# Kernel tuning notes

Hardware: AMD Instinct MI355X
Metric: run time of the kernel (lower is better)

## Reference

```python
import jax, jax.numpy as jnp
import numpy as np

B, NC, H, W = 8, 3, 24, 150
P = 2                      # patch size along time == sub_seq
WS = W // P                # 75 time segments per joint
N = H * WS                 # 1800 patches
PD = P * NC                # 6 time values per patch (time_values_per_joint)
D = 512                    # encoder_dim
L = 4                      # transformer depth
NH = 8
DH = D // NH
MLP = 4 * D
MASK_RATIO = 0.5
NM = int(MASK_RATIO * N)   # 900 masked patches


def setup_inputs() -> dict:
    key = jax.random.key(0)
    ks = jax.random.split(key, 20)
    s = 0.02
    img = jax.random.normal(ks[0], (B, NC, H, W), jnp.float32)
    valid_length = jax.random.randint(ks[1], (B,), 1, 151)
    # masked_indices = topk indices of uniform noise (matches torch.rand().topk)
    noise = jax.random.uniform(ks[2], (B, N), jnp.float32)
    masked_indices = jax.lax.top_k(noise, NM)[1]
    n = jax.random.normal
    return {
        "img": img,
        "pos_table": n(ks[3], (N + 1, D), jnp.float32) * s,
        "val_table": n(ks[4], (2, D), jnp.float32) * s,
        "patch_W": n(ks[5], (PD, D), jnp.float32) * s,
        "patch_b": jnp.zeros((D,), jnp.float32),
        "mask_token": n(ks[6], (D,), jnp.float32),
        "ln1_s": jnp.ones((L, D), jnp.float32),
        "ln1_b": jnp.zeros((L, D), jnp.float32),
        "Wqkv": n(ks[7], (L, D, 3 * D), jnp.float32) * s,
        "bqkv": jnp.zeros((L, 3 * D), jnp.float32),
        "Wo": n(ks[8], (L, D, D), jnp.float32) * s,
        "bo": jnp.zeros((L, D), jnp.float32),
        "ln2_s": jnp.ones((L, D), jnp.float32),
        "ln2_b": jnp.zeros((L, D), jnp.float32),
        "W1": n(ks[9], (L, D, MLP), jnp.float32) * s,
        "b1": jnp.zeros((L, MLP), jnp.float32),
        "W2": n(ks[10], (L, MLP, D), jnp.float32) * s,
        "b2": jnp.zeros((L, D), jnp.float32),
        "Wt": n(ks[11], (D, PD), jnp.float32) * s,
        "bt": jnp.zeros((PD,), jnp.float32),
        "valid_length": valid_length,
        "masked_indices": masked_indices,
    }


def _ln(x, s, b):
    m = jnp.mean(x, -1, keepdims=True)
    v = jnp.mean((x - m) ** 2, -1, keepdims=True)
    return (x - m) / jnp.sqrt(v + 1e-5) * s + b


def reference(img, pos_table, val_table, patch_W, patch_b, mask_token,
              ln1_s, ln1_b, Wqkv, bqkv, Wo, bo, ln2_s, ln2_b,
              W1, b1, W2, b2, Wt, bt, valid_length, masked_indices):
    # to_patch: [B,NC,H,W] -> [B, H*(W//P), P*NC]  (joint-major, time-segment inner)
    patches = jnp.transpose(img, (0, 2, 3, 1)).reshape(B, H, WS, PD).reshape(B, N, PD)

    # valid_segment construction (vectorized over batch)
    vl = jnp.where(valid_length == 150, 149, valid_length)
    n_valid = jnp.ceil(vl.astype(jnp.float32) / P).astype(jnp.int32)  # ceil(i/sub_seq)
    seg_t = (jnp.arange(WS)[None, :] < n_valid[:, None]).astype(jnp.int32)  # [B,WS]
    seg = jnp.concatenate([jnp.ones((B, 1), jnp.int32), jnp.tile(seg_t, (1, H))], axis=1)  # [B,N+1]

    pos_emb = (pos_table[None, :, :] + val_table[seg])[:, 1:]          # [B,N,D]
    tokens = patches @ patch_W + patch_b + pos_emb
    mask_toks = mask_token[None, None, :] + pos_emb

    br = jnp.arange(B)[:, None]
    bool_mask = jnp.zeros((B, N), bool).at[br, masked_indices].set(True)
    x = jnp.where(bool_mask[..., None], mask_toks, tokens)

    scale = 1.0 / np.sqrt(DH).astype(np.float32)
    for l in range(L):
        h = _ln(x, ln1_s[l], ln1_b[l])
        qkv = h @ Wqkv[l] + bqkv[l]
        q, k, v = [t.reshape(B, N, NH, DH) for t in jnp.split(qkv, 3, axis=-1)]
        att = jax.nn.softmax(jnp.einsum('bqhd,bkhd->bhqk', q, k) * scale, axis=-1)
        o = jnp.einsum('bhqk,bkhd->bqhd', att, v).reshape(B, N, D)
        x = x + o @ Wo[l] + bo[l]
        h = _ln(x, ln2_s[l], ln2_b[l])
        x = x + jax.nn.gelu(h @ W1[l] + b1[l]) @ W2[l] + b2[l]

    enc_masked = x[br, masked_indices]            # [B,NM,D]
    pred = enc_masked @ Wt + bt                   # [B,NM,PD]
    masked_patches = patches[br, masked_indices]  # [B,NM,PD]
    recon_loss = jnp.mean(jnp.abs(pred - masked_patches)) / NM
    return recon_loss
```

## Files before the change

### kernel.cpp

```cpp
#include <hip/hip_runtime.h>
#include <hip/hip_fp8.h>
#include <cstdint>

typedef _Float16 f16;
typedef _Float16 f16x2 __attribute__((ext_vector_type(2)));
typedef _Float16 f16x4 __attribute__((ext_vector_type(4)));
typedef _Float16 f16x8 __attribute__((ext_vector_type(8)));
typedef float    f32x4 __attribute__((ext_vector_type(4)));
typedef __hip_fp8_e4m3 fp8;
typedef long     i64;
typedef unsigned char u8;

#define BATCH 8
#define NSEQ  1800
#define DIM   512
#define NMASK 900
#define MROWS 14400

__device__ __forceinline__ void stage16(const void* g, void* lds_wave_base, int lane) {
#if __has_builtin(__builtin_amdgcn_global_load_lds)
  (void)lane;
  __builtin_amdgcn_global_load_lds((const __attribute__((address_space(1))) void*)g,
                                   (__attribute__((address_space(3))) void*)lds_wave_base,
                                   16, 0, 0);
#else
  ((uint4*)lds_wave_base)[lane] = *(const uint4*)g;
#endif
}

__device__ __forceinline__ float gelu_f(float x) {
  float x3 = x * x * x;
  float y  = 0.7978845608028654f * (x + 0.044715f * x3);
  float t;
  if (y > 15.f)       t = 1.f;
  else if (y < -15.f) t = -1.f;
  else { float e = __expf(2.f * y); t = (e - 1.f) / (e + 1.f); }
  return 0.5f * x * (1.f + t);
}

__global__ void scatter_mask(const int* __restrict__ mi, int* __restrict__ maskf) {
  int i = blockIdx.x * 256 + threadIdx.x;
  if (i < BATCH * NMASK) {
    int b = i / NMASK;
    maskf[b * NSEQ + mi[i]] = 1;
  }
}

__global__ void transposeW(const float* __restrict__ in, fp8* __restrict__ out, int K, int N) {
  long off = (long)blockIdx.z * K * N;
  const float* ip = in + off;
  fp8* op = out + off;
  __shared__ float tile[32][33];
  int n0 = blockIdx.x * 32, k0 = blockIdx.y * 32;
  int tx = threadIdx.x, ty = threadIdx.y;
#pragma unroll
  for (int i = 0; i < 4; ++i)
    tile[ty + 8 * i][tx] = ip[(long)(k0 + ty + 8 * i) * N + n0 + tx];
  __syncthreads();
#pragma unroll
  for (int i = 0; i < 4; ++i)
    op[(long)(n0 + ty + 8 * i) * K + k0 + tx] = fp8(tile[tx][ty + 8 * i]);
}

__global__ __launch_bounds__(256)
void transposeV(const f16* __restrict__ qkv, f16* __restrict__ Vt) {
  __shared__ f16 tl[64][72];
  const int kt = blockIdx.x, bh = blockIdx.y;
  const int b = bh >> 3, hh = bh & 7;
  const int k0 = kt * 64;
  const int t = threadIdx.x;
  const int r = t >> 3, c = t & 7;
  const f16* src = qkv + (long)b * NSEQ * 1536 + hh * 64 + 1024;
  int key0 = k0 + r;      if (key0 > NSEQ - 1) key0 = NSEQ - 1;
  int key1 = k0 + r + 32; if (key1 > NSEQ - 1) key1 = NSEQ - 1;
  *(uint4*)&tl[r][c * 8]      = *(const uint4*)(src + (long)key0 * 1536 + c * 8);
  *(uint4*)&tl[r + 32][c * 8] = *(const uint4*)(src + (long)key1 * 1536 + c * 8);
  __syncthreads();
  f16* dst = Vt + (long)bh * 64 * 1800;
  const int dh = t & 63;
#pragma unroll
  for (int it = 0; it < 2; ++it) {
    int kc = (t >> 6) + it * 4;
    if (k0 + kc * 8 < NSEQ) {
      f16x8 v;
#pragma unroll
      for (int j = 0; j < 8; ++j) v[j] = tl[kc * 8 + j][dh];
      *(f16x8*)(dst + (long)dh * 1800 + k0 + kc * 8) = v;
    }
  }
}

__global__ __launch_bounds__(256)
void prep_kernel(const float* __restrict__ img, const float* __restrict__ pos_table,
                 const float* __restrict__ val_table, const float* __restrict__ patch_W,
                 const float* __restrict__ patch_b, const float* __restrict__ mask_tok,
                 const int* __restrict__ valid_len, const int* __restrict__ maskf,
                 float* __restrict__ patches, f16* __restrict__ x0) {
  int n = blockIdx.x;
  int b = blockIdx.y;
  int t = threadIdx.x;
  __shared__ float p[6];
  int h = n / 75, ws = n % 75;
  if (t < 6) {
    int pp = t / 3, c = t % 3;
    float v = img[((b * 3 + c) * 24 + h) * 150 + ws * 2 + pp];
    p[t] = v;
    patches[((long)b * NSEQ + n) * 6 + t] = v;
  }
  __syncthreads();
  int vl = valid_len[b];
  if (vl == 150) vl = 149;
  int nv = (vl + 1) >> 1;
  int seg = (ws < nv) ? 1 : 0;
  bool masked = maskf[b * NSEQ + n] != 0;
  for (int d = t; d < DIM; d += 256) {
    float pos = pos_table[(long)(n + 1) * DIM + d] + val_table[seg * DIM + d];
    float v;
    if (masked) {
      v = mask_tok[d] + pos;
    } else {
      float acc = patch_b[d] + pos;
#pragma unroll
      for (int j = 0; j < 6; ++j) acc += p[j] * patch_W[j * DIM + d];
      v = acc;
    }
    x0[((long)b * NSEQ + n) * DIM + d] = (f16)v;
  }
}

__global__ __launch_bounds__(256)
void ln_kernel(const f16* __restrict__ x, const float* __restrict__ s,
               const float* __restrict__ bb, fp8* __restrict__ out) {
  long row = blockIdx.x;
  const f16* xr = x + row * DIM;
  int t = threadIdx.x;
  f16x2 v2 = *(const f16x2*)(xr + 2 * t);
  float v0 = (float)v2[0], v1 = (float)v2[1];
  float sum = v0 + v1, sq = v0 * v0 + v1 * v1;
#pragma unroll
  for (int mk = 1; mk < 64; mk <<= 1) {
    sum += __shfl_xor(sum, mk);
    sq  += __shfl_xor(sq, mk);
  }
  __shared__ float red[8];
  int wave = t >> 6, lane = t & 63;
  if (lane == 0) { red[wave] = sum; red[wave + 4] = sq; }
  __syncthreads();
  sum = red[0] + red[1] + red[2] + red[3];
  sq  = red[4] + red[5] + red[6] + red[7];
  float mean = sum * (1.f / DIM);
  float var  = sq * (1.f / DIM) - mean * mean;
  float rstd = rsqrtf(var + 1e-5f);
  fp8 o2[2];
  o2[0] = fp8((v0 - mean) * rstd * s[2 * t]     + bb[2 * t]);
  o2[1] = fp8((v1 - mean) * rstd * s[2 * t + 1] + bb[2 * t + 1]);
  *(uint16_t*)&out[row * DIM + 2 * t] = *(const uint16_t*)o2;
}

template <int EPI>
__global__ __launch_bounds__(256)
void gemm8_kernel(const u8* __restrict__ A, const u8* __restrict__ Bt,
                  const float* __restrict__ bias, const f16* __restrict__ res,
                  f16* __restrict__ outH, fp8* __restrict__ out8,
                  int M, int N, int K, int gx) {
  __shared__ u8 As[8 * 128 * 16];
  __shared__ u8 Bs[8 * 128 * 16];
  const int tid  = threadIdx.x;
  const int wave = tid >> 6, lane = tid & 63;
  const int quad = lane >> 4, l16 = lane & 15;
  const int wm = wave >> 1, wn = wave & 1;

  const int nwg = (int)gridDim.x;
  const int q = nwg >> 3, rr = nwg & 7;
  const int xcd = (int)blockIdx.x & 7, idx = (int)blockIdx.x >> 3;
  const int wg = (xcd < rr ? xcd * (q + 1) : rr * (q + 1) + (xcd - rr) * q) + idx;
  const long rowBase = (long)(wg / gx) * 128;
  const long colBase = (long)(wg % gx) * 128;

  f32x4 acc[4][4];
  f32x4 zero = {0.f, 0.f, 0.f, 0.f};
#pragma unroll
  for (int ni = 0; ni < 4; ++ni)
#pragma unroll
    for (int mi = 0; mi < 4; ++mi) acc[ni][mi] = zero;

  long rA0 = rowBase + lane;       if (rA0 > M - 1) rA0 = M - 1;
  long rA1 = rowBase + 64 + lane;  if (rA1 > M - 1) rA1 = M - 1;
  const u8* Arow0 = A + rA0 * K + wave * 16;
  const u8* Arow1 = A + rA1 * K + wave * 16;
  const u8* Brow0 = Bt + (colBase + lane) * K + wave * 16;
  const u8* Brow1 = Bt + (colBase + 64 + lane) * K + wave * 16;
  u8* AsC0 = As + wave * 2048;
  u8* AsC1 = AsC0 + 64 * 16;
  u8* AsC2 = As + (wave + 4) * 2048;
  u8* AsC3 = AsC2 + 64 * 16;
  u8* BsC0 = Bs + wave * 2048;
  u8* BsC1 = BsC0 + 64 * 16;
  u8* BsC2 = Bs + (wave + 4) * 2048;
  u8* BsC3 = BsC2 + 64 * 16;

  for (int kt = 0; kt < K; kt += 128) {
    __syncthreads();
    stage16(Arow0 + kt,      AsC0, lane);
    stage16(Arow1 + kt,      AsC1, lane);
    stage16(Arow0 + kt + 64, AsC2, lane);
    stage16(Arow1 + kt + 64, AsC3, lane);
    stage16(Brow0 + kt,      BsC0, lane);
    stage16(Brow1 + kt,      BsC1, lane);
    stage16(Brow0 + kt + 64, BsC2, lane);
    stage16(Brow1 + kt + 64, BsC3, lane);
    __syncthreads();
#pragma unroll
    for (int ks = 0; ks < 4; ++ks) {
      const int cb = (2 * ks + (quad >> 1)) * 2048 + (quad & 1) * 8;
      i64 af[4], bf[4];
#pragma unroll
      for (int mi = 0; mi < 4; ++mi)
        af[mi] = *(const i64*)&As[cb + (wm * 64 + mi * 16 + l16) * 16];
#pragma unroll
      for (int ni = 0; ni < 4; ++ni)
        bf[ni] = *(const i64*)&Bs[cb + (wn * 64 + ni * 16 + l16) * 16];
#pragma unroll
      for (int ni = 0; ni < 4; ++ni)
#pragma unroll
        for (int mi = 0; mi < 4; ++mi)
          acc[ni][mi] = __builtin_amdgcn_mfma_f32_16x16x32_fp8_fp8(bf[ni], af[mi], acc[ni][mi], 0, 0, 0);
    }
  }

#pragma unroll
  for (int mi = 0; mi < 4; ++mi) {
    long m = rowBase + wm * 64 + mi * 16 + l16;
    if (m < M) {
#pragma unroll
      for (int ni = 0; ni < 4; ++ni) {
        long n = colBase + wn * 64 + ni * 16 + quad * 4;
        float4 bv = *(const float4*)&bias[n];
        f32x4 v = acc[ni][mi];
        v[0] += bv.x; v[1] += bv.y; v[2] += bv.z; v[3] += bv.w;
        long o = m * N + n;
        if (EPI == 1) {
          f16x4 rr4 = *(const f16x4*)&res[o];
          f16x4 ov;
#pragma unroll
          for (int r = 0; r < 4; ++r) ov[r] = (f16)(v[r] + (float)rr4[r]);
          *(f16x4*)&outH[o] = ov;
        } else if (EPI == 2) {
          fp8 hv[4];
#pragma unroll
          for (int r = 0; r < 4; ++r) hv[r] = fp8(gelu_f(v[r]));
          *(uint32_t*)&out8[o] = *(const uint32_t*)hv;
        } else {
          f16x4 hv;
#pragma unroll
          for (int r = 0; r < 4; ++r) hv[r] = (f16)v[r];
          *(f16x4*)&outH[o] = hv;
        }
      }
    }
  }
}

#define ATTN_TILE_BODY(MASKV)                                                           \
  {                                                                                     \
    _Pragma("unroll")                                                                   \
    for (int n = 0; n < 4; ++n) {                                                       \
      f16x8 b0 = *(const f16x8*)&Ks[n * 16 + l16][quad * 8];                            \
      f16x8 b1 = *(const f16x8*)&Ks[n * 16 + l16][32 + quad * 8];                       \
      f32x4 zz = {0.f, 0.f, 0.f, 0.f};                                                  \
      zz = __builtin_amdgcn_mfma_f32_16x16x32_f16(qfA0, b0, zz, 0, 0, 0);               \
      zz = __builtin_amdgcn_mfma_f32_16x16x32_f16(qfA1, b1, zz, 0, 0, 0);               \
      bool bad = (MASKV) && (n > 0 || l16 >= 8);                                        \
      _Pragma("unroll")                                                                 \
      for (int r = 0; r < 4; ++r) {                                                     \
        float pp = exp2f(fmaf(zz[r], K1, -8.f));                                        \
        if (bad) pp = 0.f;                                                              \
        Ps[wave * 16 + quad * 4 + r][n * 16 + l16] = (f16)pp;                           \
        lsA[r] += pp;                                                                   \
      }                                                                                 \
    }                                                                                   \
    {                                                                                   \
      f16x8 pa0 = *(const f16x8*)&Ps[wave * 16 + l16][quad * 8];                        \
      f16x8 pa1 = *(const f16x8*)&Ps[wave * 16 + l16][32 + quad * 8];                   \
      _Pragma("unroll")                                                                 \
      for (int nt = 0; nt < 4; ++nt) {                                                  \
        f16x8 vb0 = *(const f16x8*)&Vs[nt * 16 + l16][quad * 8];                        \
        f16x8 vb1 = *(const f16x8*)&Vs[nt * 16 + l16][32 + quad * 8];                   \
        oA[nt] = __builtin_amdgcn_mfma_f32_16x16x32_f16(pa0, vb0, oA[nt], 0, 0, 0);     \
        oA[nt] = __builtin_amdgcn_mfma_f32_16x16x32_f16(pa1, vb1, oA[nt], 0, 0, 0);     \
      }                                                                                 \
    }                                                                                   \
    _Pragma("unroll")                                                                   \
    for (int n = 0; n < 4; ++n) {                                                       \
      f16x8 b0 = *(const f16x8*)&Ks[n * 16 + l16][quad * 8];                            \
      f16x8 b1 = *(const f16x8*)&Ks[n * 16 + l16][32 + quad * 8];                       \
      f32x4 zz = {0.f, 0.f, 0.f, 0.f};                                                  \
      zz = __builtin_amdgcn_mfma_f32_16x16x32_f16(qfB0, b0, zz, 0, 0, 0);               \
      zz = __builtin_amdgcn_mfma_f32_16x16x32_f16(qfB1, b1, zz, 0, 0, 0);               \
      bool bad = (MASKV) && (n > 0 || l16 >= 8);                                        \
      _Pragma("unroll")                                                                 \
      for (int r = 0; r < 4; ++r) {                                                     \
        float pp = exp2f(fmaf(zz[r], K1, -8.f));                                        \
        if (bad) pp = 0.f;                                                              \
        Ps[wave * 16 + quad * 4 + r][n * 16 + l16] = (f16)pp;                           \
        lsB[r] += pp;                                                                   \
      }                                                                                 \
    }                                                                                   \
    {                                                                                   \
      f16x8 pa0 = *(const f16x8*)&Ps[wave * 16 + l16][quad * 8];                        \
      f16x8 pa1 = *(const f16x8*)&Ps[wave * 16 + l16][32 + quad * 8];                   \
      _Pragma("unroll")                                                                 \
      for (int nt = 0; nt < 4; ++nt) {                                                  \
        f16x8 vb0 = *(const f16x8*)&Vs[nt * 16 + l16][quad * 8];                        \
        f16x8 vb1 = *(const f16x8*)&Vs[nt * 16 + l16][32 + quad * 8];                   \
        oB[nt] = __builtin_amdgcn_mfma_f32_16x16x32_f16(pa0, vb0, oB[nt], 0, 0, 0);     \
        oB[nt] = __builtin_amdgcn_mfma_f32_16x16x32_f16(pa1, vb1, oB[nt], 0, 0, 0);     \
      }                                                                                 \
    }                                                                                   \
  }

__global__ __launch_bounds__(256, 4)
void attn_kernel(const f16* __restrict__ qkv, const f16* __restrict__ Vt,
                 fp8* __restrict__ out) {
  const int g = blockIdx.x;
  const int hi = g / 120, rem = g % 120;
  const int qt = rem >> 3;
  const int bh = hi * 8 + (rem & 7);
  const int b = bh >> 3, hh = bh & 7;
  const int t = threadIdx.x;
  const int wave = t >> 6, lane = t & 63;
  const int quad = lane >> 4, l16 = lane & 15;
  const int q0 = qt * 128;
  const long baseBN = (long)b * NSEQ;
  const float K1 = 0.18033688011112042f;

  __shared__ f16 Ks[64][80];
  __shared__ f16 Vs[64][80];
  __shared__ f16 Ps[64][80];

  int qrA = q0 + wave * 32 + l16;      if (qrA > NSEQ - 1) qrA = NSEQ - 1;
  int qrB = q0 + wave * 32 + 16 + l16; if (qrB > NSEQ - 1) qrB = NSEQ - 1;
  const f16* QpA = qkv + (baseBN + qrA) * 1536 + hh * 64 + quad * 8;
  const f16* QpB = qkv + (baseBN + qrB) * 1536 + hh * 64 + quad * 8;
  f16x8 qfA0 = *(const f16x8*)(QpA);
  f16x8 qfA1 = *(const f16x8*)(QpA + 32);
  f16x8 qfB0 = *(const f16x8*)(QpB);
  f16x8 qfB1 = *(const f16x8*)(QpB + 32);

  f32x4 oA[4], oB[4];
  float lsA[4] = {0.f, 0.f, 0.f, 0.f}, lsB[4] = {0.f, 0.f, 0.f, 0.f};
#pragma unroll
  for (int nt = 0; nt < 4; ++nt) { oA[nt] = f32x4{0,0,0,0}; oB[nt] = f32x4{0,0,0,0}; }

  const f16* Kg = qkv + baseBN * 1536 + hh * 64 + 512;
  const f16* Vg = Vt + (long)bh * 64 * 1800;
  const int sr = t >> 3, sc = t & 7;
  const uint4 z4 = {0u, 0u, 0u, 0u};

  const f16* KgS = Kg + (long)sr * 1536 + sc * 8;
  const f16* VgS = Vg + (long)sr * 1800 + sc * 8;

  uint4 pk0 = *(const uint4*)(KgS);
  uint4 pk1 = *(const uint4*)(KgS + (long)32 * 1536);
  uint4 pv0 = *(const uint4*)(VgS);
  uint4 pv1 = *(const uint4*)(VgS + (long)32 * 1800);

  for (int kt = 0; kt < 28; ++kt) {
    __syncthreads();
    *(uint4*)&Ks[sr][sc * 8]      = pk0;
    *(uint4*)&Ks[sr + 32][sc * 8] = pk1;
    *(uint4*)&Vs[sr][sc * 8]      = pv0;
    *(uint4*)&Vs[sr + 32][sc * 8] = pv1;
    {
      long ko = (long)(kt + 1) * 64;
      pk0 = *(const uint4*)(KgS + ko * 1536);
      pk1 = *(const uint4*)(KgS + (ko + 32) * 1536);
      bool vok = (ko + sc * 8) < NSEQ;
      pv0 = vok ? *(const uint4*)(VgS + ko) : z4;
      pv1 = vok ? *(const uint4*)(VgS + (long)32 * 1800 + ko) : z4;
    }
    __syncthreads();
    ATTN_TILE_BODY(false)
  }
  {
    __syncthreads();
    *(uint4*)&Ks[sr][sc * 8]      = pk0;
    *(uint4*)&Ks[sr + 32][sc * 8] = pk1;
    *(uint4*)&Vs[sr][sc * 8]      = pv0;
    *(uint4*)&Vs[sr + 32][sc * 8] = pv1;
    __syncthreads();
    ATTN_TILE_BODY(true)
  }

#pragma unroll
  for (int mk = 1; mk < 16; mk <<= 1)
#pragma unroll
    for (int r = 0; r < 4; ++r) {
      lsA[r] += __shfl_xor(lsA[r], mk);
      lsB[r] += __shfl_xor(lsB[r], mk);
    }

#pragma unroll
  for (int r = 0; r < 4; ++r) {
    int qgA = q0 + wave * 32 + quad * 4 + r;
    if (qgA < NSEQ) {
      float inv = 1.f / lsA[r];
#pragma unroll
      for (int nt = 0; nt < 4; ++nt)
        out[(baseBN + qgA) * 512 + hh * 64 + nt * 16 + l16] = fp8(oA[nt][r] * inv);
    }
    int qgB = qgA + 16;
    if (qgB < NSEQ) {
      float inv = 1.f / lsB[r];
#pragma unroll
      for (int nt = 0; nt < 4; ++nt)
        out[(baseBN + qgB) * 512 + hh * 64 + nt * 16 + l16] = fp8(oB[nt][r] * inv);
    }
  }
}

__global__ __launch_bounds__(192)
void head_kernel(const f16* __restrict__ x, const float* __restrict__ patches,
                 const int* __restrict__ mi, const float* __restrict__ Wt,
                 const float* __restrict__ bt, float* __restrict__ lossAcc) {
  int t = threadIdx.x;
  int pd = t / 32, sg = t % 32;
  float wt[16];
#pragma unroll
  for (int k = 0; k < 16; ++k) wt[k] = Wt[(sg * 16 + k) * 6 + pd];
  float btv = bt[pd];
  float accAll = 0.f;
  for (int rr = 0; rr < 32; ++rr) {
    int bi = blockIdx.x * 32 + rr;
    int b = bi / NMASK;
    int idx = mi[bi];
    const f16x8* xr8 = (const f16x8*)(x + ((long)b * NSEQ + idx) * DIM);
    float acc = 0.f;
#pragma unroll
    for (int j = 0; j < 2; ++j) {
      f16x8 xa = xr8[sg * 2 + j];
#pragma unroll
      for (int k2 = 0; k2 < 8; ++k2) acc += (float)xa[k2] * wt[j * 8 + k2];
    }
#pragma unroll
    for (int mk = 1; mk < 32; mk <<= 1) acc += __shfl_xor(acc, mk);
    if (sg == 0) {
      float pred = acc + btv;
      accAll += fabsf(pred - patches[((long)b * NSEQ + idx) * 6 + pd]);
    }
  }
  if (sg == 0) atomicAdd(lossAcc, accAll);
}

__global__ void finalize_kernel(const float* __restrict__ acc, float* __restrict__ out) {
  if (threadIdx.x == 0 && blockIdx.x == 0)
    out[0] = acc[0] * (1.0f / 38880000.0f);
}

extern "C" void kernel_launch(void* const* d_in, const int* in_sizes, int n_in,
                              void* d_out, int out_size, void* d_ws, size_t ws_size,
                              hipStream_t stream) {
  (void)in_sizes; (void)n_in; (void)out_size; (void)ws_size;
  const float* img       = (const float*)d_in[0];
  const float* pos_table = (const float*)d_in[1];
  const float* val_table = (const float*)d_in[2];
  const float* patch_W   = (const float*)d_in[3];
  const float* patch_b   = (const float*)d_in[4];
  const float* mask_tok  = (const float*)d_in[5];
  const float* ln1_s     = (const float*)d_in[6];
  const float* ln1_b     = (const float*)d_in[7];
  const float* Wqkv      = (const float*)d_in[8];
  const float* bqkv      = (const float*)d_in[9];
  const float* Wo        = (const float*)d_in[10];
  const float* bo        = (const float*)d_in[11];
  const float* ln2_s     = (const float*)d_in[12];
  const float* ln2_b     = (const float*)d_in[13];
  const float* W1        = (const float*)d_in[14];
  const float* b1        = (const float*)d_in[15];
  const float* W2        = (const float*)d_in[16];
  const float* b2        = (const float*)d_in[17];
  const float* Wt        = (const float*)d_in[18];
  const float* bt        = (const float*)d_in[19];
  const int* valid_len   = (const int*)d_in[20];
  const int* mask_idx    = (const int*)d_in[21];

  char* p = (char*)d_ws;
  auto alloc = [&](size_t bytes) { char* r = p; p += (bytes + 511) & ~(size_t)511; return r; };
  float* patches = (float*)alloc((size_t)MROWS * 6 * 4);
  int*   maskf   = (int*)alloc((size_t)MROWS * 4);
  float* lossAcc = (float*)alloc(256);
  f16*   x       = (f16*)alloc((size_t)MROWS * 512 * 2);
  char*  hbuf    = alloc((size_t)MROWS * 512 * 2 + 512);
  f16*   qkv     = (f16*)alloc((size_t)MROWS * 2048 * 2);
  fp8*   attn    = (fp8*)alloc((size_t)MROWS * 512);
  fp8*   WqT     = (fp8*)alloc((size_t)4 * 1536 * 512);
  fp8*   WoT     = (fp8*)alloc((size_t)4 * 512 * 512);
  fp8*   W1T     = (fp8*)alloc((size_t)4 * 2048 * 512);
  fp8*   W2T     = (fp8*)alloc((size_t)4 * 512 * 2048);
  fp8*   h       = (fp8*)hbuf;
  f16*   Vt      = (f16*)hbuf;
  fp8*   hid     = (fp8*)qkv;

  hipMemsetAsync(maskf, 0, (size_t)MROWS * 4, stream);
  hipMemsetAsync(lossAcc, 0, 4, stream);
  scatter_mask<<<29, 256, 0, stream>>>(mask_idx, maskf);

  transposeW<<<dim3(48, 16, 4), dim3(32, 8), 0, stream>>>(Wqkv, WqT, 512, 1536);
  transposeW<<<dim3(16, 16, 4), dim3(32, 8), 0, stream>>>(Wo,  WoT, 512, 512);
  transposeW<<<dim3(64, 16, 4), dim3(32, 8), 0, stream>>>(W1,  W1T, 512, 2048);
  transposeW<<<dim3(16, 64, 4), dim3(32, 8), 0, stream>>>(W2,  W2T, 2048, 512);

  prep_kernel<<<dim3(1800, 8), 256, 0, stream>>>(img, pos_table, val_table, patch_W, patch_b,
                                                 mask_tok, valid_len, maskf, patches, x);

  for (int l = 0; l < 4; ++l) {
    ln_kernel<<<MROWS, 256, 0, stream>>>(x, ln1_s + l * 512, ln1_b + l * 512, h);
    gemm8_kernel<0><<<dim3(12 * 113), 256, 0, stream>>>((const u8*)h, (const u8*)(WqT + (size_t)l * 1536 * 512),
                                                        bqkv + l * 1536, nullptr, qkv, nullptr,
                                                        MROWS, 1536, 512, 12);
    transposeV<<<dim3(29, 64), 256, 0, stream>>>(qkv, Vt);
    attn_kernel<<<dim3(960), 256, 0, stream>>>(qkv, Vt, attn);
    gemm8_kernel<1><<<dim3(4 * 113), 256, 0, stream>>>((const u8*)attn, (const u8*)(WoT + (size_t)l * 512 * 512),
                                                       bo + l * 512, x, x, nullptr,
                                                       MROWS, 512, 512, 4);
    ln_kernel<<<MROWS, 256, 0, stream>>>(x, ln2_s + l * 512, ln2_b + l * 512, h);
    gemm8_kernel<2><<<dim3(16 * 113), 256, 0, stream>>>((const u8*)h, (const u8*)(W1T + (size_t)l * 2048 * 512),
                                                        b1 + l * 2048, nullptr, nullptr, hid,
                                                        MROWS, 2048, 512, 16);
    gemm8_kernel<1><<<dim3(4 * 113), 256, 0, stream>>>((const u8*)hid, (const u8*)(W2T + (size_t)l * 512 * 2048),
                                                       b2 + l * 512, x, x, nullptr,
                                                       MROWS, 512, 2048, 4);
  }

  head_kernel<<<225, 192, 0, stream>>>(x, patches, mask_idx, Wt, bt, lossAcc);
  finalize_kernel<<<1, 64, 0, stream>>>(lossAcc, (float*)d_out);
}
```

Baseline: 1.472 ms.

## Fuse V transpose into QKV GEMM epilogue and batch rows per LayerNorm block

The QKV GEMM epilogue now writes the V columns straight into the transposed Vt layout, so the separate transposeV kernel and its round trip through the qkv buffer go away. Vt gets its own workspace buffer because it can no longer alias the LayerNorm output. LayerNorm now processes 8 rows per block, one wave per two rows, with vectorized 8-element loads and wave-only reductions. This cuts block count and removes shared-memory synchronization. The fused V store is strided by NSEQ per element and uncoalesced, which may make the GEMM epilogue slower.

```diff
diff --git a/kernel.cpp b/kernel.cpp
--- a/kernel.cpp
+++ b/kernel.cpp
@@ -60,34 +60,6 @@
 #pragma unroll
   for (int i = 0; i < 4; ++i)
     op[(long)(n0 + ty + 8 * i) * K + k0 + tx] = fp8(tile[tx][ty + 8 * i]);
-}
-
-__global__ __launch_bounds__(256)
-void transposeV(const f16* __restrict__ qkv, f16* __restrict__ Vt) {
-  __shared__ f16 tl[64][72];
-  const int kt = blockIdx.x, bh = blockIdx.y;
-  const int b = bh >> 3, hh = bh & 7;
-  const int k0 = kt * 64;
-  const int t = threadIdx.x;
-  const int r = t >> 3, c = t & 7;
-  const f16* src = qkv + (long)b * NSEQ * 1536 + hh * 64 + 1024;
-  int key0 = k0 + r;      if (key0 > NSEQ - 1) key0 = NSEQ - 1;
-  int key1 = k0 + r + 32; if (key1 > NSEQ - 1) key1 = NSEQ - 1;
-  *(uint4*)&tl[r][c * 8]      = *(const uint4*)(src + (long)key0 * 1536 + c * 8);
-  *(uint4*)&tl[r + 32][c * 8] = *(const uint4*)(src + (long)key1 * 1536 + c * 8);
-  __syncthreads();
-  f16* dst = Vt + (long)bh * 64 * 1800;
-  const int dh = t & 63;
-#pragma unroll
-  for (int it = 0; it < 2; ++it) {
-    int kc = (t >> 6) + it * 4;
-    if (k0 + kc * 8 < NSEQ) {
-      f16x8 v;
-#pragma unroll
-      for (int j = 0; j < 8; ++j) v[j] = tl[kc * 8 + j][dh];
-      *(f16x8*)(dst + (long)dh * 1800 + k0 + kc * 8) = v;
-    }
-  }
 }
 
 __global__ __launch_bounds__(256)
@@ -131,37 +103,46 @@
 __global__ __launch_bounds__(256)
 void ln_kernel(const f16* __restrict__ x, const float* __restrict__ s,
                const float* __restrict__ bb, fp8* __restrict__ out) {
-  long row = blockIdx.x;
-  const f16* xr = x + row * DIM;
-  int t = threadIdx.x;
-  f16x2 v2 = *(const f16x2*)(xr + 2 * t);
-  float v0 = (float)v2[0], v1 = (float)v2[1];
-  float sum = v0 + v1, sq = v0 * v0 + v1 * v1;
-#pragma unroll
-  for (int mk = 1; mk < 64; mk <<= 1) {
-    sum += __shfl_xor(sum, mk);
-    sq  += __shfl_xor(sq, mk);
-  }
-  __shared__ float red[8];
-  int wave = t >> 6, lane = t & 63;
-  if (lane == 0) { red[wave] = sum; red[wave + 4] = sq; }
-  __syncthreads();
-  sum = red[0] + red[1] + red[2] + red[3];
-  sq  = red[4] + red[5] + red[6] + red[7];
-  float mean = sum * (1.f / DIM);
-  float var  = sq * (1.f / DIM) - mean * mean;
-  float rstd = rsqrtf(var + 1e-5f);
-  fp8 o2[2];
-  o2[0] = fp8((v0 - mean) * rstd * s[2 * t]     + bb[2 * t]);
-  o2[1] = fp8((v1 - mean) * rstd * s[2 * t + 1] + bb[2 * t + 1]);
-  *(uint16_t*)&out[row * DIM + 2 * t] = *(const uint16_t*)o2;
+  const int t = threadIdx.x;
+  const int wave = t >> 6, lane = t & 63;
+  const int col = lane * 8;
+  float sv[8], bv[8];
+  {
+    float4 s0 = *(const float4*)&s[col], s1 = *(const float4*)&s[col + 4];
+    float4 b0 = *(const float4*)&bb[col], b1 = *(const float4*)&bb[col + 4];
+    sv[0] = s0.x; sv[1] = s0.y; sv[2] = s0.z; sv[3] = s0.w;
+    sv[4] = s1.x; sv[5] = s1.y; sv[6] = s1.z; sv[7] = s1.w;
+    bv[0] = b0.x; bv[1] = b0.y; bv[2] = b0.z; bv[3] = b0.w;
+    bv[4] = b1.x; bv[5] = b1.y; bv[6] = b1.z; bv[7] = b1.w;
+  }
+  long rowBase = (long)blockIdx.x * 8 + wave * 2;
+#pragma unroll
+  for (int rr = 0; rr < 2; ++rr) {
+    long row = rowBase + rr;
+    f16x8 v = *(const f16x8*)(x + row * DIM + col);
+    float f[8], sum = 0.f, sq = 0.f;
+#pragma unroll
+    for (int j = 0; j < 8; ++j) { f[j] = (float)v[j]; sum += f[j]; sq += f[j] * f[j]; }
+#pragma unroll
+    for (int mk = 1; mk < 64; mk <<= 1) {
+      sum += __shfl_xor(sum, mk);
+      sq  += __shfl_xor(sq, mk);
+    }
+    float mean = sum * (1.f / DIM);
+    float var  = sq * (1.f / DIM) - mean * mean;
+    float rstd = rsqrtf(var + 1e-5f);
+    fp8 o8[8];
+#pragma unroll
+    for (int j = 0; j < 8; ++j) o8[j] = fp8((f[j] - mean) * rstd * sv[j] + bv[j]);
+    *(uint2*)&out[row * DIM + col] = *(const uint2*)o8;
+  }
 }
 
 template <int EPI>
 __global__ __launch_bounds__(256)
 void gemm8_kernel(const u8* __restrict__ A, const u8* __restrict__ Bt,
                   const float* __restrict__ bias, const f16* __restrict__ res,
-                  f16* __restrict__ outH, fp8* __restrict__ out8,
+                  f16* __restrict__ outH, fp8* __restrict__ out8, f16* __restrict__ outV,
                   int M, int N, int K, int gx) {
   __shared__ u8 As[8 * 128 * 16];
   __shared__ u8 Bs[8 * 128 * 16];
@@ -226,6 +207,29 @@
         for (int mi = 0; mi < 4; ++mi)
           acc[ni][mi] = __builtin_amdgcn_mfma_f32_16x16x32_fp8_fp8(bf[ni], af[mi], acc[ni][mi], 0, 0, 0);
     }
+  }
+
+  if (EPI == 0 && outV != nullptr && colBase >= 1024) {
+    const int hh = (int)((colBase - 1024) >> 6) + wn;
+#pragma unroll
+    for (int mi = 0; mi < 4; ++mi) {
+      long m = rowBase + wm * 64 + mi * 16 + l16;
+      if (m < M) {
+        int b = (int)m / NSEQ;
+        int key = (int)m - b * NSEQ;
+        f16* vdst = outV + ((long)(b * 8 + hh) * 64) * NSEQ + key;
+#pragma unroll
+        for (int ni = 0; ni < 4; ++ni) {
+          long n = colBase + wn * 64 + ni * 16 + quad * 4;
+          float4 bv = *(const float4*)&bias[n];
+          f32x4 v = acc[ni][mi];
+#pragma unroll
+          for (int r = 0; r < 4; ++r)
+            vdst[(long)(ni * 16 + quad * 4 + r) * NSEQ] = (f16)(v[r] + (&bv.x)[r]);
+        }
+      }
+    }
+    return;
   }
 
 #pragma unroll
@@ -490,15 +494,14 @@
   int*   maskf   = (int*)alloc((size_t)MROWS * 4);
   float* lossAcc = (float*)alloc(256);
   f16*   x       = (f16*)alloc((size_t)MROWS * 512 * 2);
-  char*  hbuf    = alloc((size_t)MROWS * 512 * 2 + 512);
+  fp8*   h       = (fp8*)alloc((size_t)MROWS * 512 + 512);
+  f16*   Vt      = (f16*)alloc((size_t)64 * 64 * 1800 * 2 + 512);
   f16*   qkv     = (f16*)alloc((size_t)MROWS * 2048 * 2);
   fp8*   attn    = (fp8*)alloc((size_t)MROWS * 512);
   fp8*   WqT     = (fp8*)alloc((size_t)4 * 1536 * 512);
   fp8*   WoT     = (fp8*)alloc((size_t)4 * 512 * 512);
   fp8*   W1T     = (fp8*)alloc((size_t)4 * 2048 * 512);
   fp8*   W2T     = (fp8*)alloc((size_t)4 * 512 * 2048);
-  fp8*   h       = (fp8*)hbuf;
-  f16*   Vt      = (f16*)hbuf;
   fp8*   hid     = (fp8*)qkv;
 
   hipMemsetAsync(maskf, 0, (size_t)MROWS * 4, stream);
@@ -514,21 +517,20 @@
                                                  mask_tok, valid_len, maskf, patches, x);
 
   for (int l = 0; l < 4; ++l) {
-    ln_kernel<<<MROWS, 256, 0, stream>>>(x, ln1_s + l * 512, ln1_b + l * 512, h);
+    ln_kernel<<<1800, 256, 0, stream>>>(x, ln1_s + l * 512, ln1_b + l * 512, h);
     gemm8_kernel<0><<<dim3(12 * 113), 256, 0, stream>>>((const u8*)h, (const u8*)(WqT + (size_t)l * 1536 * 512),
-                                                        bqkv + l * 1536, nullptr, qkv, nullptr,
+                                                        bqkv + l * 1536, nullptr, qkv, nullptr, Vt,
                                                         MROWS, 1536, 512, 12);
-    transposeV<<<dim3(29, 64), 256, 0, stream>>>(qkv, Vt);
     attn_kernel<<<dim3(960), 256, 0, stream>>>(qkv, Vt, attn);
     gemm8_kernel<1><<<dim3(4 * 113), 256, 0, stream>>>((const u8*)attn, (const u8*)(WoT + (size_t)l * 512 * 512),
-                                                       bo + l * 512, x, x, nullptr,
+                                                       bo + l * 512, x, x, nullptr, nullptr,
                                                        MROWS, 512, 512, 4);
-    ln_kernel<<<MROWS, 256, 0, stream>>>(x, ln2_s + l * 512, ln2_b + l * 512, h);
+    ln_kernel<<<1800, 256, 0, stream>>>(x, ln2_s + l * 512, ln2_b + l * 512, h);
     gemm8_kernel<2><<<dim3(16 * 113), 256, 0, stream>>>((const u8*)h, (const u8*)(W1T + (size_t)l * 2048 * 512),
-                                                        b1 + l * 2048, nullptr, nullptr, hid,
+                                                        b1 + l * 2048, nullptr, nullptr, hid, nullptr,
                                                         MROWS, 2048, 512, 16);
     gemm8_kernel<1><<<dim3(4 * 113), 256, 0, stream>>>((const u8*)hid, (const u8*)(W2T + (size_t)l * 512 * 2048),
-                                                       b2 + l * 512, x, x, nullptr,
+                                                       b2 + l * 512, x, x, nullptr, nullptr,
                                                        MROWS, 512, 2048, 4);
   }
 
```

Result: faster. 1.396 ms (-5.1%).
